# Kernel optimization log

Hardware: AMD Instinct MI355X
Metric: run time of the kernel (lower is better)

Reference implementation:

```python
import jax, jax.numpy as jnp
import numpy as np

SP = 4      # sp_size (number of simulated sequence-parallel ranks)
NH = 16     # num_attention_heads
HD = 64     # head_dim
HS = 1024   # hidden_size
B = 1       # batch
S = 8192    # global sequence length (SP chunks of 2048)


def setup_inputs() -> dict:
    key = jax.random.key(0)
    ks = jax.random.split(key, 9)
    w_scale = 1.0 / np.sqrt(HS)
    def w(k):
        # xavier-ish init, stored as [in, out] so y = x @ W + b
        return jax.random.uniform(k, (HS, HS), jnp.float32, -w_scale, w_scale)
    return {
        'hidden_states': jax.random.normal(ks[0], (B, S, HS), jnp.float32),
        'Wq': w(ks[1]), 'bq': jnp.zeros((HS,), jnp.float32),
        'Wk': w(ks[2]), 'bk': jnp.zeros((HS,), jnp.float32),
        'Wv': w(ks[3]), 'bv': jnp.zeros((HS,), jnp.float32),
        'Wo': w(ks[4]), 'bo': jnp.zeros((HS,), jnp.float32),
    }


def reference(hidden_states, Wq, bq, Wk, bk, Wv, bv, Wo, bo):
    b, s, _ = hidden_states.shape
    sc = s // SP  # per-rank chunk length
    inv_sqrt_hd = 1.0 / np.sqrt(HD)

    def heads(x):
        # [B, S, HS] -> [SP, B, NH, Sc, HD]
        return x.reshape(b, SP, sc, NH, HD).transpose(1, 0, 3, 2, 4)

    q = heads(hidden_states @ Wq + bq)
    k = heads(hidden_states @ Wk + bk)
    v = heads(hidden_states @ Wv + bv)

    out = jnp.zeros_like(q)
    # ring attention: at step i each rank r attends to chunk (r + i) mod SP
    for i in range(SP):
        ki = jnp.roll(k, -i, axis=0)
        vi = jnp.roll(v, -i, axis=0)
        scores = jnp.einsum('sbhqd,sbhkd->sbhqk', q, ki) * inv_sqrt_hd
        probs = jax.nn.softmax(scores, axis=-1)  # per-chunk softmax (faithful to source)
        out = out + jnp.einsum('sbhqk,sbhkd->sbhqd', probs, vi)
    out = out / SP  # source divides accumulated context by sp_size

    # [SP, B, NH, Sc, HD] -> [B, S, NH*HD]
    ctx = out.transpose(1, 0, 3, 2, 4).reshape(b, s, NH * HD)
    return ctx @ Wo + bo
```

## Files before the change

kernel.cpp:

```cpp
#include <hip/hip_runtime.h>

#define DEVINL __device__ __forceinline__

typedef __attribute__((ext_vector_type(8))) short short8;
typedef __attribute__((ext_vector_type(4))) float floatx4;
typedef __attribute__((ext_vector_type(2))) unsigned uintx2;

DEVINL unsigned short f2bf(float f){
  unsigned u = __builtin_bit_cast(unsigned, f);
  u += 0x7FFFu + ((u >> 16) & 1u);
  return (unsigned short)(u >> 16);
}
DEVINL unsigned pk2(float a, float b){
  unsigned ua = __builtin_bit_cast(unsigned, a);
  unsigned ub = __builtin_bit_cast(unsigned, b);
  ua += 0x7FFFu + ((ua >> 16) & 1u);
  ub += 0x7FFFu + ((ub >> 16) & 1u);
  return (ua >> 16) | (ub & 0xFFFF0000u);
}
DEVINL unsigned pkfast(float a, float b){
  unsigned ua = __builtin_bit_cast(unsigned, a) + 0x8000u;
  unsigned ub = __builtin_bit_cast(unsigned, b) + 0x8000u;
  return __builtin_amdgcn_perm(ub, ua, 0x07060302u);
}
DEVINL float bf2f(unsigned short h){
  unsigned u = ((unsigned)h) << 16;
  return __builtin_bit_cast(float, u);
}
DEVINL void gload_lds16(const void* g, void* l){
  __builtin_amdgcn_global_load_lds((const __attribute__((address_space(1))) void*)g,
                                   (__attribute__((address_space(3))) void*)l, 16, 0, 0);
}
DEVINL int perm2(int k){
  return (((k >> 4) & 1) << 5) | (((k >> 2) & 3) << 3) | (((k >> 5) & 1) << 2) | (k & 3);
}

__global__ void k_detect(const unsigned* __restrict__ w, int* __restrict__ flag){
  __shared__ int cnt;
  if (threadIdx.x == 0) cnt = 0;
  __syncthreads();
  int c = 0;
  for (int i = threadIdx.x; i < 1024; i += 256){
    unsigned e = (w[i] >> 7) & 0xFFu;
    c += (e >= 120u && e <= 132u) ? 1 : 0;
  }
  atomicAdd(&cnt, c);
  __syncthreads();
  if (threadIdx.x == 0) *flag = (cnt > 512) ? 1 : 0;
}

__global__ void k_conv_bf16(const void* __restrict__ src, unsigned short* __restrict__ dst,
                            int n, const int* __restrict__ flag){
  int i = (blockIdx.x * 256 + threadIdx.x) * 8;
  if (i >= n) return;
  if (*flag){
    ((uint4*)dst)[i >> 3] = ((const uint4*)src)[i >> 3];
  } else {
    const float* s = (const float*)src;
    short8 v;
    #pragma unroll
    for (int j = 0; j < 8; j++) v[j] = (short)f2bf(s[i + j]);
    *(short8*)(dst + i) = v;
  }
}

__global__ void k_conv_wT(const void* __restrict__ src, unsigned short* __restrict__ dst,
                          const int* __restrict__ flag){
  __shared__ float tile[32][33];
  const int tx = threadIdx.x & 31, ty = threadIdx.x >> 5;
  const int bx = blockIdx.x, by = blockIdx.y;
  const int isbf = *flag;
  #pragma unroll
  for (int r = 0; r < 32; r += 8){
    int k = by*32 + ty + r, n = bx*32 + tx;
    float v = isbf ? bf2f(((const unsigned short*)src)[k*1024 + n])
                   : ((const float*)src)[k*1024 + n];
    tile[ty + r][tx] = v;
  }
  __syncthreads();
  #pragma unroll
  for (int r = 0; r < 32; r += 8){
    int n = bx*32 + ty + r, k = by*32 + tx;
    dst[n*1024 + k] = f2bf(tile[tx][ty + r]);
  }
}

__global__ void k_conv_f32(const void* __restrict__ src, float* __restrict__ dst,
                           int n, const int* __restrict__ flag){
  int i = blockIdx.x * 256 + threadIdx.x;
  if (i >= n) return;
  dst[i] = (*flag) ? bf2f(((const unsigned short*)src)[i]) : ((const float*)src)[i];
}

template<int MODE>
__global__ __launch_bounds__(256, 2) void k_gemm(
    const unsigned short* __restrict__ A, const unsigned short* __restrict__ Bt,
    const float* __restrict__ bias, void* __restrict__ C0, void* __restrict__ C1,
    void* __restrict__ C2, const int* __restrict__ flagp, float scale)
{
  const int K = 1024;
  __shared__ __align__(16) unsigned short As[128*32];
  __shared__ __align__(16) unsigned short Bs[128*32];
  const int tid = threadIdx.x;
  const int lane = tid & 63, wave = tid >> 6;
  const int quad = lane >> 4, l15 = lane & 15;
  const int m0 = blockIdx.x * 128, n0 = blockIdx.y * 128;
  const int wm = (wave >> 1) * 64, wn = (wave & 1) * 64;
  const floatx4 fzero = {0.f, 0.f, 0.f, 0.f};
  floatx4 acc[4][4];
  #pragma unroll
  for (int i = 0; i < 4; i++)
    #pragma unroll
    for (int j = 0; j < 4; j++) acc[i][j] = fzero;

  for (int k0 = 0; k0 < K; k0 += 32){
    __syncthreads();
    #pragma unroll
    for (int rep = 0; rep < 2; rep++){
      int idx = tid + rep*256;
      int row = idx >> 2, c = idx & 3;
      gload_lds16(A  + (size_t)(m0 + row)*K + (k0 + c*8), &As[idx*8]);
      gload_lds16(Bt + (size_t)(n0 + row)*K + (k0 + c*8), &Bs[idx*8]);
    }
    asm volatile("s_waitcnt vmcnt(0)" ::: "memory");
    __syncthreads();
    short8 af[4], bf[4];
    #pragma unroll
    for (int i = 0; i < 4; i++) af[i] = *(const short8*)&As[(wm + i*16 + l15)*32 + quad*8];
    #pragma unroll
    for (int j = 0; j < 4; j++) bf[j] = *(const short8*)&Bs[(wn + j*16 + l15)*32 + quad*8];
    #pragma unroll
    for (int i = 0; i < 4; i++)
      #pragma unroll
      for (int j = 0; j < 4; j++)
        acc[i][j] = __builtin_amdgcn_mfma_f32_16x16x32_bf16(af[i], bf[j], acc[i][j], 0, 0, 0);
  }

  float bs[4];
  #pragma unroll
  for (int j = 0; j < 4; j++) bs[j] = bias[n0 + wn + j*16 + l15];
  const int useBf = (MODE == 1) ? *flagp : 1;
  #pragma unroll
  for (int i = 0; i < 4; i++){
    #pragma unroll
    for (int j = 0; j < 4; j++){
      int n = n0 + wn + j*16 + l15;
      #pragma unroll
      for (int r = 0; r < 4; r++){
        int m = m0 + wm + i*16 + quad*4 + r;
        float v = acc[i][j][r] + bs[j];
        if (MODE == 3){
          int sel = n >> 10, nn = n & 1023;
          if (sel == 0){
            ((unsigned short*)C0)[((size_t)(nn >> 6)*8192 + m)*64 + (nn & 63)] = f2bf(v * scale);
          } else if (sel == 1){
            ((unsigned short*)C1)[((size_t)(nn >> 6)*8192 + m)*64 + (nn & 63)] = f2bf(v);
          } else {
            ((unsigned short*)C2)[(size_t)nn*8192 + ((m & ~63) | perm2(m & 63))] = f2bf(v);
          }
        } else {
          if (useBf) ((unsigned short*)C0)[(size_t)m*1024 + n] = f2bf(v);
          else       ((float*)C0)[(size_t)m*1024 + n] = v;
        }
      }
    }
  }
}

__global__ __launch_bounds__(256, 2) void k_attn(
    const unsigned short* __restrict__ Qg, const unsigned short* __restrict__ Kg,
    const unsigned short* __restrict__ Vg, unsigned short* __restrict__ ctx)
{
  __shared__ __align__(16) unsigned short Qs[256*64];
  __shared__ __align__(16) unsigned short Ks[2][64*64];
  __shared__ __align__(16) unsigned short Vs[2][64*64];
  const int tid = threadIdx.x, lane = tid & 63, wave = tid >> 6;
  const int quad = lane >> 4, l15 = lane & 15;
  const int bid = blockIdx.x;
  const int xcd = bid & 7, slot = bid >> 3;
  const int h = xcd*2 + (slot >> 5);
  const int rem = slot & 31, rchunk = rem >> 3, qt = rem & 7;
  const int sq0 = rchunk*2048 + qt*256;
  const unsigned short* Qh = Qg + (size_t)h*8192*64;
  const unsigned short* Kh = Kg + (size_t)h*8192*64;
  const unsigned short* Vh = Vg + (size_t)h*8192*64;
  const int wq0 = wave * 64;
  const floatx4 fzero = {0.f, 0.f, 0.f, 0.f};

  #pragma unroll
  for (int rep = 0; rep < 8; rep++){
    int idx = tid + rep*256, row = idx >> 3, c = idx & 7;
    short8 v = *(const short8*)(Qh + (size_t)(sq0 + row)*64 + c*8);
    *(short8*)&Qs[row*64 + (c ^ (row & 7))*8] = v;
  }
  __syncthreads();
  short8 qf[4][2];
  #pragma unroll
  for (int mi = 0; mi < 4; mi++)
    #pragma unroll
    for (int ks = 0; ks < 2; ks++){
      int row = wq0 + mi*16 + l15;
      qf[mi][ks] = *(const short8*)&Qs[row*64 + (((ks*4 + quad) ^ (row & 7)))*8];
    }

  short8 tk[2], tv[2];
  auto loadKV = [&](int t){
    int ci = (t >> 5) & 3;
    int kvs = ((rchunk + ci) & 3)*2048 + (t & 31)*64;
    #pragma unroll
    for (int rep = 0; rep < 2; rep++){
      int idx = tid + rep*256, row = idx >> 3, c = idx & 7;
      tk[rep] = *(const short8*)(Kh + (size_t)(kvs + row)*64 + c*8);
      tv[rep] = *(const short8*)(Vh + (size_t)row*8192 + kvs + c*8);
    }
  };
  auto storeKV = [&](int buf){
    #pragma unroll
    for (int rep = 0; rep < 2; rep++){
      int idx = tid + rep*256, row = idx >> 3, c = idx & 7;
      int pos = row*64 + (c ^ (row & 7))*8;
      *(short8*)&Ks[buf][pos] = tk[rep];
      *(short8*)&Vs[buf][pos] = tv[rep];
    }
  };

  loadKV(0);
  storeKV(0);

  floatx4 Of[4][4];
  #pragma unroll
  for (int mi = 0; mi < 4; mi++)
    #pragma unroll
    for (int di = 0; di < 4; di++) Of[mi][di] = fzero;

  for (int i = 0; i < 4; i++){
    float lacc[4] = {0.f, 0.f, 0.f, 0.f};
    floatx4 Oc[4][4];
    #pragma unroll
    for (int mi = 0; mi < 4; mi++)
      #pragma unroll
      for (int di = 0; di < 4; di++) Oc[mi][di] = fzero;

    for (int kt = 0; kt < 32; kt++){
      const int t = i*32 + kt, cur = t & 1;
      __syncthreads();
      {
        int nt = (t + 1 < 128) ? (t + 1) : 127;
        loadKV(nt);
      }

      short8 pf[4][2];
      #pragma unroll
      for (int mi = 0; mi < 4; mi++){
        floatx4 St[4];
        #pragma unroll
        for (int ni = 0; ni < 4; ni++) St[ni] = fzero;
        #pragma unroll
        for (int ks = 0; ks < 2; ks++)
          #pragma unroll
          for (int ni = 0; ni < 4; ni++){
            int krow = ni*16 + l15;
            short8 kf = *(const short8*)&Ks[cur][krow*64 + (((ks*4 + quad) ^ (krow & 7)))*8];
            St[ni] = __builtin_amdgcn_mfma_f32_16x16x32_bf16(kf, qf[mi][ks], St[ni], 0, 0, 0);
          }
        float part = 0.f;
        #pragma unroll
        for (int ni = 0; ni < 4; ni++)
          #pragma unroll
          for (int r = 0; r < 4; r++){
            St[ni][r] = __builtin_amdgcn_exp2f(St[ni][r]);
            part += St[ni][r];
          }
        lacc[mi] += part;
        #pragma unroll
        for (int ks = 0; ks < 2; ks++){
          uintx2 lo, hi;
          lo[0] = pkfast(St[ks  ][0], St[ks  ][1]);
          lo[1] = pkfast(St[ks  ][2], St[ks  ][3]);
          hi[0] = pkfast(St[2+ks][0], St[2+ks][1]);
          hi[1] = pkfast(St[2+ks][2], St[2+ks][3]);
          union { uintx2 u[2]; short8 s; } cv;
          cv.u[0] = lo; cv.u[1] = hi;
          pf[mi][ks] = cv.s;
        }
      }

      #pragma unroll
      for (int ks = 0; ks < 2; ks++)
        #pragma unroll
        for (int di = 0; di < 4; di++){
          int vrow = di*16 + l15;
          short8 vf = *(const short8*)&Vs[cur][vrow*64 + (((ks*4 + quad) ^ (vrow & 7)))*8];
          #pragma unroll
          for (int mi = 0; mi < 4; mi++)
            Oc[mi][di] = __builtin_amdgcn_mfma_f32_16x16x32_bf16(vf, pf[mi][ks], Oc[mi][di], 0, 0, 0);
        }

      storeKV(cur ^ 1);
    }

    #pragma unroll
    for (int mi = 0; mi < 4; mi++){
      float ls = lacc[mi];
      ls += __shfl_xor(ls, 16);
      ls += __shfl_xor(ls, 32);
      float inv = __builtin_amdgcn_rcpf(ls);
      #pragma unroll
      for (int di = 0; di < 4; di++)
        #pragma unroll
        for (int r = 0; r < 4; r++) Of[mi][di][r] += Oc[mi][di][r] * inv;
    }
  }

  #pragma unroll
  for (int mi = 0; mi < 4; mi++){
    int q = sq0 + wq0 + mi*16 + l15;
    #pragma unroll
    for (int di = 0; di < 4; di++){
      uintx2 w;
      w[0] = pk2(Of[mi][di][0]*0.25f, Of[mi][di][1]*0.25f);
      w[1] = pk2(Of[mi][di][2]*0.25f, Of[mi][di][3]*0.25f);
      *(uintx2*)&ctx[(size_t)q*1024 + h*64 + di*16 + quad*4] = w;
    }
  }
}

extern "C" void kernel_launch(void* const* d_in, const int* in_sizes, int n_in,
                              void* d_out, int out_size, void* d_ws, size_t ws_size,
                              hipStream_t stream)
{
  (void)in_sizes; (void)n_in; (void)out_size; (void)ws_size;
  char* ws = (char*)d_ws;
  size_t off = 0;
  auto alloc = [&](size_t bytes) -> char* {
    char* p = ws + off;
    off = (off + bytes + 255) & ~(size_t)255;
    return p;
  };
  int* flag            = (int*)alloc(4);
  unsigned short* hsb  = (unsigned short*)alloc((size_t)8192*1024*2);
  unsigned short* wqt  = (unsigned short*)alloc((size_t)1024*1024*2);
  unsigned short* wkt  = (unsigned short*)alloc((size_t)1024*1024*2);
  unsigned short* wvt  = (unsigned short*)alloc((size_t)1024*1024*2);
  unsigned short* wot  = (unsigned short*)alloc((size_t)1024*1024*2);
  float* bqf           = (float*)alloc(1024*4);
  float* bkf           = (float*)alloc(1024*4);
  float* bvf           = (float*)alloc(1024*4);
  float* bof           = (float*)alloc(1024*4);
  unsigned short* Qb   = (unsigned short*)alloc((size_t)16*8192*64*2);
  unsigned short* Kb   = (unsigned short*)alloc((size_t)16*8192*64*2);
  unsigned short* Vb   = (unsigned short*)alloc((size_t)16*8192*64*2);
  unsigned short* ctxb = (unsigned short*)alloc((size_t)8192*1024*2);

  k_detect<<<1, 256, 0, stream>>>((const unsigned*)d_in[0], flag);
  k_conv_bf16<<<4096, 256, 0, stream>>>(d_in[0], hsb, 8192*1024, flag);
  k_conv_wT<<<dim3(32,32), 256, 0, stream>>>(d_in[1], wqt, flag);
  k_conv_wT<<<dim3(32,32), 256, 0, stream>>>(d_in[3], wkt, flag);
  k_conv_wT<<<dim3(32,32), 256, 0, stream>>>(d_in[5], wvt, flag);
  k_conv_wT<<<dim3(32,32), 256, 0, stream>>>(d_in[7], wot, flag);
  k_conv_f32<<<4, 256, 0, stream>>>(d_in[2], bqf, 1024, flag);
  k_conv_f32<<<4, 256, 0, stream>>>(d_in[4], bkf, 1024, flag);
  k_conv_f32<<<4, 256, 0, stream>>>(d_in[6], bvf, 1024, flag);
  k_conv_f32<<<4, 256, 0, stream>>>(d_in[8], bof, 1024, flag);

  const float Cs = 0.18033688011112042f;
  k_gemm<3><<<dim3(64, 24), 256, 0, stream>>>(hsb, wqt, bqf, Qb, Kb, Vb, nullptr, Cs);

  k_attn<<<512, 256, 0, stream>>>(Qb, Kb, Vb, ctxb);

  k_gemm<1><<<dim3(64, 8), 256, 0, stream>>>(ctxb, wot, bof, d_out, nullptr, nullptr, flag, 1.0f);
}
```

Baseline: 521.1 us.

## Use direct global-to-LDS loads in attention with pre-swizzled QKV layout

The QKV projection GEMM now writes Q, K and V already XOR-swizzled, so the attention kernel can stage tiles with direct global-to-LDS 16-byte loads instead of going through registers and storing to LDS. The per-row softmax denominator now comes from an extra MFMA against a vector of ones instead of scalar adds and cross-lane shuffles. The four weight-transpose launches and four bias launches are each merged into a single launch. This cuts VGPR pressure and store instructions in the attention loop, but adds a vmcnt(0) wait before every barrier and extra MFMA work.

```diff
diff --git a/kernel.cpp b/kernel.cpp
--- a/kernel.cpp
+++ b/kernel.cpp
@@ -64,9 +64,19 @@
   }
 }
 
-__global__ void k_conv_wT(const void* __restrict__ src, unsigned short* __restrict__ dst,
-                          const int* __restrict__ flag){
+__global__ void k_conv_wT4(const void* __restrict__ s0, const void* __restrict__ s1,
+                           const void* __restrict__ s2, const void* __restrict__ s3,
+                           unsigned short* __restrict__ d0, unsigned short* __restrict__ d1,
+                           unsigned short* __restrict__ d2, unsigned short* __restrict__ d3,
+                           const int* __restrict__ flag){
   __shared__ float tile[32][33];
+  const void* src; unsigned short* dst;
+  switch (blockIdx.z){
+    case 0: src = s0; dst = d0; break;
+    case 1: src = s1; dst = d1; break;
+    case 2: src = s2; dst = d2; break;
+    default: src = s3; dst = d3; break;
+  }
   const int tx = threadIdx.x & 31, ty = threadIdx.x >> 5;
   const int bx = blockIdx.x, by = blockIdx.y;
   const int isbf = *flag;
@@ -85,11 +95,14 @@
   }
 }
 
-__global__ void k_conv_f32(const void* __restrict__ src, float* __restrict__ dst,
-                           int n, const int* __restrict__ flag){
+__global__ void k_conv_b4(const void* __restrict__ s0, const void* __restrict__ s1,
+                          const void* __restrict__ s2, const void* __restrict__ s3,
+                          float* __restrict__ dst, const int* __restrict__ flag){
   int i = blockIdx.x * 256 + threadIdx.x;
-  if (i >= n) return;
-  dst[i] = (*flag) ? bf2f(((const unsigned short*)src)[i]) : ((const float*)src)[i];
+  if (i >= 4096) return;
+  int z = i >> 10, j = i & 1023;
+  const void* s = (z == 0) ? s0 : (z == 1) ? s1 : (z == 2) ? s2 : s3;
+  dst[i] = (*flag) ? bf2f(((const unsigned short*)s)[j]) : ((const float*)s)[j];
 }
 
 template<int MODE>
@@ -152,11 +165,14 @@
         if (MODE == 3){
           int sel = n >> 10, nn = n & 1023;
           if (sel == 0){
-            ((unsigned short*)C0)[((size_t)(nn >> 6)*8192 + m)*64 + (nn & 63)] = f2bf(v * scale);
+            int dd = (nn & 63) ^ ((m & 7) << 3);
+            ((unsigned short*)C0)[((size_t)(nn >> 6)*8192 + m)*64 + dd] = f2bf(v * scale);
           } else if (sel == 1){
-            ((unsigned short*)C1)[((size_t)(nn >> 6)*8192 + m)*64 + (nn & 63)] = f2bf(v);
+            int dd = (nn & 63) ^ ((m & 7) << 3);
+            ((unsigned short*)C1)[((size_t)(nn >> 6)*8192 + m)*64 + dd] = f2bf(v);
           } else {
-            ((unsigned short*)C2)[(size_t)nn*8192 + ((m & ~63) | perm2(m & 63))] = f2bf(v);
+            int s2 = perm2(m & 63) ^ ((nn & 7) << 3);
+            ((unsigned short*)C2)[(size_t)nn*8192 + (m & ~63) + s2] = f2bf(v);
           }
         } else {
           if (useBf) ((unsigned short*)C0)[(size_t)m*1024 + n] = f2bf(v);
@@ -181,19 +197,36 @@
   const int h = xcd*2 + (slot >> 5);
   const int rem = slot & 31, rchunk = rem >> 3, qt = rem & 7;
   const int sq0 = rchunk*2048 + qt*256;
-  const unsigned short* Qh = Qg + (size_t)h*8192*64;
-  const unsigned short* Kh = Kg + (size_t)h*8192*64;
-  const unsigned short* Vh = Vg + (size_t)h*8192*64;
+  const char* Qbase = (const char*)(Qg + (size_t)h*8192*64 + (size_t)sq0*64);
+  const char* Kbase = (const char*)(Kg + (size_t)h*8192*64);
+  const char* Vbase = (const char*)(Vg + (size_t)h*8192*64);
   const int wq0 = wave * 64;
   const floatx4 fzero = {0.f, 0.f, 0.f, 0.f};
 
+  const int idx0 = tid, idx1 = tid + 256;
+  const size_t voff0 = (size_t)(idx0 >> 3)*16384 + (idx0 & 7)*16;
+  const size_t voff1 = (size_t)(idx1 >> 3)*16384 + (idx1 & 7)*16;
+
+  auto stage = [&](int buf, int kvs){
+    const char* Kt = Kbase + (size_t)kvs*128;
+    const char* Vt = Vbase + (size_t)kvs*2;
+    char* kd = (char*)Ks[buf];
+    char* vd = (char*)Vs[buf];
+    gload_lds16(Kt + idx0*16, kd + idx0*16);
+    gload_lds16(Kt + idx1*16, kd + idx1*16);
+    gload_lds16(Vt + voff0, vd + idx0*16);
+    gload_lds16(Vt + voff1, vd + idx1*16);
+  };
+
   #pragma unroll
   for (int rep = 0; rep < 8; rep++){
-    int idx = tid + rep*256, row = idx >> 3, c = idx & 7;
-    short8 v = *(const short8*)(Qh + (size_t)(sq0 + row)*64 + c*8);
-    *(short8*)&Qs[row*64 + (c ^ (row & 7))*8] = v;
-  }
+    int idx = tid + rep*256;
+    gload_lds16(Qbase + idx*16, (char*)Qs + idx*16);
+  }
+  stage(0, rchunk*2048);
+  asm volatile("s_waitcnt vmcnt(0)" ::: "memory");
   __syncthreads();
+
   short8 qf[4][2];
   #pragma unroll
   for (int mi = 0; mi < 4; mi++)
@@ -203,29 +236,9 @@
       qf[mi][ks] = *(const short8*)&Qs[row*64 + (((ks*4 + quad) ^ (row & 7)))*8];
     }
 
-  short8 tk[2], tv[2];
-  auto loadKV = [&](int t){
-    int ci = (t >> 5) & 3;
-    int kvs = ((rchunk + ci) & 3)*2048 + (t & 31)*64;
-    #pragma unroll
-    for (int rep = 0; rep < 2; rep++){
-      int idx = tid + rep*256, row = idx >> 3, c = idx & 7;
-      tk[rep] = *(const short8*)(Kh + (size_t)(kvs + row)*64 + c*8);
-      tv[rep] = *(const short8*)(Vh + (size_t)row*8192 + kvs + c*8);
-    }
-  };
-  auto storeKV = [&](int buf){
-    #pragma unroll
-    for (int rep = 0; rep < 2; rep++){
-      int idx = tid + rep*256, row = idx >> 3, c = idx & 7;
-      int pos = row*64 + (c ^ (row & 7))*8;
-      *(short8*)&Ks[buf][pos] = tk[rep];
-      *(short8*)&Vs[buf][pos] = tv[rep];
-    }
-  };
-
-  loadKV(0);
-  storeKV(0);
+  short8 ones;
+  #pragma unroll
+  for (int j = 0; j < 8; j++) ones[j] = (short)0x3F80;
 
   floatx4 Of[4][4];
   #pragma unroll
@@ -234,19 +247,22 @@
     for (int di = 0; di < 4; di++) Of[mi][di] = fzero;
 
   for (int i = 0; i < 4; i++){
-    float lacc[4] = {0.f, 0.f, 0.f, 0.f};
-    floatx4 Oc[4][4];
-    #pragma unroll
-    for (int mi = 0; mi < 4; mi++)
+    floatx4 Oc[4][4], Ol[4];
+    #pragma unroll
+    for (int mi = 0; mi < 4; mi++){
+      Ol[mi] = fzero;
       #pragma unroll
       for (int di = 0; di < 4; di++) Oc[mi][di] = fzero;
+    }
 
     for (int kt = 0; kt < 32; kt++){
       const int t = i*32 + kt, cur = t & 1;
+      asm volatile("s_waitcnt vmcnt(0)" ::: "memory");
       __syncthreads();
-      {
-        int nt = (t + 1 < 128) ? (t + 1) : 127;
-        loadKV(nt);
+      if (t < 127){
+        int t1 = t + 1;
+        int kvs = ((rchunk + (t1 >> 5)) & 3)*2048 + (t1 & 31)*64;
+        stage(cur ^ 1, kvs);
       }
 
       short8 pf[4][2];
@@ -263,15 +279,11 @@
             short8 kf = *(const short8*)&Ks[cur][krow*64 + (((ks*4 + quad) ^ (krow & 7)))*8];
             St[ni] = __builtin_amdgcn_mfma_f32_16x16x32_bf16(kf, qf[mi][ks], St[ni], 0, 0, 0);
           }
-        float part = 0.f;
         #pragma unroll
         for (int ni = 0; ni < 4; ni++)
           #pragma unroll
-          for (int r = 0; r < 4; r++){
+          for (int r = 0; r < 4; r++)
             St[ni][r] = __builtin_amdgcn_exp2f(St[ni][r]);
-            part += St[ni][r];
-          }
-        lacc[mi] += part;
         #pragma unroll
         for (int ks = 0; ks < 2; ks++){
           uintx2 lo, hi;
@@ -286,7 +298,7 @@
       }
 
       #pragma unroll
-      for (int ks = 0; ks < 2; ks++)
+      for (int ks = 0; ks < 2; ks++){
         #pragma unroll
         for (int di = 0; di < 4; di++){
           int vrow = di*16 + l15;
@@ -295,16 +307,15 @@
           for (int mi = 0; mi < 4; mi++)
             Oc[mi][di] = __builtin_amdgcn_mfma_f32_16x16x32_bf16(vf, pf[mi][ks], Oc[mi][di], 0, 0, 0);
         }
-
-      storeKV(cur ^ 1);
+        #pragma unroll
+        for (int mi = 0; mi < 4; mi++)
+          Ol[mi] = __builtin_amdgcn_mfma_f32_16x16x32_bf16(ones, pf[mi][ks], Ol[mi], 0, 0, 0);
+      }
     }
 
     #pragma unroll
     for (int mi = 0; mi < 4; mi++){
-      float ls = lacc[mi];
-      ls += __shfl_xor(ls, 16);
-      ls += __shfl_xor(ls, 32);
-      float inv = __builtin_amdgcn_rcpf(ls);
+      float inv = __builtin_amdgcn_rcpf(Ol[mi][0]);
       #pragma unroll
       for (int di = 0; di < 4; di++)
         #pragma unroll
@@ -343,10 +354,7 @@
   unsigned short* wkt  = (unsigned short*)alloc((size_t)1024*1024*2);
   unsigned short* wvt  = (unsigned short*)alloc((size_t)1024*1024*2);
   unsigned short* wot  = (unsigned short*)alloc((size_t)1024*1024*2);
-  float* bqf           = (float*)alloc(1024*4);
-  float* bkf           = (float*)alloc(1024*4);
-  float* bvf           = (float*)alloc(1024*4);
-  float* bof           = (float*)alloc(1024*4);
+  float* biasAll       = (float*)alloc(4096*4);
   unsigned short* Qb   = (unsigned short*)alloc((size_t)16*8192*64*2);
   unsigned short* Kb   = (unsigned short*)alloc((size_t)16*8192*64*2);
   unsigned short* Vb   = (unsigned short*)alloc((size_t)16*8192*64*2);
@@ -354,19 +362,15 @@
 
   k_detect<<<1, 256, 0, stream>>>((const unsigned*)d_in[0], flag);
   k_conv_bf16<<<4096, 256, 0, stream>>>(d_in[0], hsb, 8192*1024, flag);
-  k_conv_wT<<<dim3(32,32), 256, 0, stream>>>(d_in[1], wqt, flag);
-  k_conv_wT<<<dim3(32,32), 256, 0, stream>>>(d_in[3], wkt, flag);
-  k_conv_wT<<<dim3(32,32), 256, 0, stream>>>(d_in[5], wvt, flag);
-  k_conv_wT<<<dim3(32,32), 256, 0, stream>>>(d_in[7], wot, flag);
-  k_conv_f32<<<4, 256, 0, stream>>>(d_in[2], bqf, 1024, flag);
-  k_conv_f32<<<4, 256, 0, stream>>>(d_in[4], bkf, 1024, flag);
-  k_conv_f32<<<4, 256, 0, stream>>>(d_in[6], bvf, 1024, flag);
-  k_conv_f32<<<4, 256, 0, stream>>>(d_in[8], bof, 1024, flag);
+  k_conv_wT4<<<dim3(32,32,4), 256, 0, stream>>>(d_in[1], d_in[3], d_in[5], d_in[7],
+                                                wqt, wkt, wvt, wot, flag);
+  k_conv_b4<<<16, 256, 0, stream>>>(d_in[2], d_in[4], d_in[6], d_in[8], biasAll, flag);
 
   const float Cs = 0.18033688011112042f;
-  k_gemm<3><<<dim3(64, 24), 256, 0, stream>>>(hsb, wqt, bqf, Qb, Kb, Vb, nullptr, Cs);
+  k_gemm<3><<<dim3(64, 24), 256, 0, stream>>>(hsb, wqt, biasAll, Qb, Kb, Vb, nullptr, Cs);
 
   k_attn<<<512, 256, 0, stream>>>(Qb, Kb, Vb, ctxb);
 
-  k_gemm<1><<<dim3(64, 8), 256, 0, stream>>>(ctxb, wot, bof, d_out, nullptr, nullptr, flag, 1.0f);
-}
+  k_gemm<1><<<dim3(64, 8), 256, 0, stream>>>(ctxb, wot, biasAll + 3072, d_out,
+                                             nullptr, nullptr, flag, 1.0f);
+}
```

New measurement: 472.9 us. 9.2% less time.
